# Optimization experiments

Measured on AMD Instinct MI355X. Metric: run time of the kernel, lower is better.

The kernel has to match this reference:

```python
import jax, jax.numpy as jnp
import numpy as np

B, S, H = 4096, 64, 256
NUM_STEPS = 200
DT = 0.01


def setup_inputs() -> dict:
    key = jax.random.key(0)
    ks = jax.random.split(key, 7)
    sc = lambda fan_in: 1.0 / np.sqrt(fan_in)
    return {
        "x0": jax.random.normal(ks[0], (B, S), dtype=jnp.float32),
        "W1": jax.random.normal(ks[1], (S, H), dtype=jnp.float32) * sc(S),
        "b1": jax.random.normal(ks[2], (H,), dtype=jnp.float32) * sc(S),
        "W2": jax.random.normal(ks[3], (H, H), dtype=jnp.float32) * sc(H),
        "b2": jax.random.normal(ks[4], (H,), dtype=jnp.float32) * sc(H),
        "W3": jax.random.normal(ks[5], (H, S), dtype=jnp.float32) * sc(H),
        "b3": jax.random.normal(ks[6], (S,), dtype=jnp.float32) * sc(H),
        "dt_scale": jnp.ones((1,), dtype=jnp.float32) * 0.01,
        "num_steps": NUM_STEPS,
    }


def reference(x0, W1, b1, W2, b2, W3, b3, dt_scale, num_steps):
    # Euler integration of dx/dt = MLP(x); trajectory = [x0, x1, ..., x_num_steps]
    def step(x, _):
        h = jnp.tanh(x @ W1 + b1)          # [B, H]
        h = jnp.tanh(h @ W2 + b2)          # [B, H]
        dx_dt = h @ W3 + b3                # [B, S]
        x_next = x + dx_dt * dt_scale * DT
        return x_next, x_next

    _, traj = jax.lax.scan(step, x0, None, length=num_steps)  # [T, B, S]
    traj = jnp.moveaxis(traj, 0, 1)                            # [B, T, S]
    return jnp.concatenate([x0[:, None, :], traj], axis=1)     # [B, T+1, S]
```

## Files before the change

### kernel.cpp

```cpp
#include <hip/hip_runtime.h>
#include <hip/hip_bf16.h>

typedef __bf16 bf16x8 __attribute__((ext_vector_type(8)));
typedef __bf16 bf16x4 __attribute__((ext_vector_type(4)));
typedef float  f32x4  __attribute__((ext_vector_type(4)));

__device__ __forceinline__ float fast_tanh(float x) {
    float e = __expf(2.0f * x);
    float r = __builtin_amdgcn_rcpf(e + 1.0f);
    return __builtin_fmaf(-2.0f, r, 1.0f);
}

__global__ void prep_weights(const float* __restrict__ W1,
                             const float* __restrict__ W2,
                             const float* __restrict__ W3,
                             __bf16* __restrict__ w1t,
                             __bf16* __restrict__ w2t,
                             __bf16* __restrict__ w3t) {
    int idx = blockIdx.x * blockDim.x + threadIdx.x;
    if (idx < 64 * 256) {
        int n = idx >> 6, k = idx & 63;
        w1t[idx] = (__bf16)W1[k * 256 + n];
    }
    int i2 = idx - 64 * 256;
    if (i2 >= 0 && i2 < 256 * 256) {
        int n = i2 >> 8, k = i2 & 255;
        w2t[i2] = (__bf16)W2[k * 256 + n];
    }
    int i3 = idx - 64 * 256 - 256 * 256;
    if (i3 >= 0 && i3 < 64 * 256) {
        int n = i3 >> 8, k = i3 & 255;
        w3t[i3] = (__bf16)W3[k * 64 + n];
    }
}

__global__ __launch_bounds__(512, 2)
void ode_kernel(const float* __restrict__ x0,
                const float* __restrict__ b1,
                const float* __restrict__ b2,
                const float* __restrict__ b3,
                const float* __restrict__ dt_scale,
                const int*   __restrict__ num_steps,
                const __bf16* __restrict__ w1t,
                const __bf16* __restrict__ w2t,
                const __bf16* __restrict__ w3t,
                float* __restrict__ out) {
    __shared__ float  xs[16][68];
    __shared__ __bf16 xb[16][72];
    __shared__ __bf16 h1[16][264];
    __shared__ __bf16 h2[16][264];

    const int tid  = threadIdx.x;
    const int wave = tid >> 6;
    const int lane = tid & 63;
    const int q    = lane >> 4;
    const int c    = lane & 15;
    const int row0 = blockIdx.x * 16;

    const float scale = dt_scale[0] * 0.01f;
    const int   nT    = num_steps[0];

    bf16x8 w1f[2][2];
    #pragma unroll
    for (int kt = 0; kt < 2; ++kt)
        #pragma unroll
        for (int nt = 0; nt < 2; ++nt) {
            int n = wave * 32 + nt * 16 + c;
            w1f[kt][nt] = *(const bf16x8*)(w1t + n * 64 + kt * 32 + q * 8);
        }
    bf16x8 w2f[8][2];
    #pragma unroll
    for (int kt = 0; kt < 8; ++kt)
        #pragma unroll
        for (int nt = 0; nt < 2; ++nt) {
            int n = wave * 32 + nt * 16 + c;
            w2f[kt][nt] = *(const bf16x8*)(w2t + n * 256 + kt * 32 + q * 8);
        }
    bf16x8 w3f[8];
    f32x4  b3v4 = (f32x4){0.f, 0.f, 0.f, 0.f};
    if (wave < 4) {
        int n = wave * 16 + c;
        #pragma unroll
        for (int kt = 0; kt < 8; ++kt)
            w3f[kt] = *(const bf16x8*)(w3t + n * 256 + kt * 32 + q * 8);
        b3v4 = *(const f32x4*)(b3 + wave * 16 + q * 4);
    }
    f32x4 b1v4[2], b2v4[2];
    #pragma unroll
    for (int nt = 0; nt < 2; ++nt) {
        b1v4[nt] = *(const f32x4*)(b1 + wave * 32 + nt * 16 + q * 4);
        b2v4[nt] = *(const f32x4*)(b2 + wave * 32 + nt * 16 + q * 4);
    }

    const int mio = tid >> 5, sio = (tid & 31) * 2;
    float* outp = out + ((size_t)(row0 + mio) * 201) * 64 + sio;
    {
        const float2 v = *(const float2*)(x0 + (size_t)(row0 + mio) * 64 + sio);
        xs[mio][sio]     = v.x;  xs[mio][sio + 1] = v.y;
        xb[mio][sio]     = (__bf16)v.x;
        xb[mio][sio + 1] = (__bf16)v.y;
        *(float2*)outp = v;
        outp += 64;
    }
    __syncthreads();

    for (int t = 0; t < nT; ++t) {
        {
            f32x4 acc[2] = {b1v4[0], b1v4[1]};
            #pragma unroll
            for (int kt = 0; kt < 2; ++kt) {
                bf16x8 a = *(const bf16x8*)(&xb[c][kt * 32 + q * 8]);
                acc[0] = __builtin_amdgcn_mfma_f32_16x16x32_bf16(w1f[kt][0], a, acc[0], 0, 0, 0);
                acc[1] = __builtin_amdgcn_mfma_f32_16x16x32_bf16(w1f[kt][1], a, acc[1], 0, 0, 0);
            }
            #pragma unroll
            for (int nt = 0; nt < 2; ++nt) {
                bf16x4 o;
                #pragma unroll
                for (int r = 0; r < 4; ++r) o[r] = (__bf16)fast_tanh(acc[nt][r]);
                *(bf16x4*)(&h1[c][wave * 32 + nt * 16 + q * 4]) = o;
            }
        }
        __syncthreads();

        {
            f32x4 acc[2]  = {b2v4[0], b2v4[1]};
            f32x4 accB[2] = {(f32x4){0,0,0,0}, (f32x4){0,0,0,0}};
            #pragma unroll
            for (int kt = 0; kt < 4; ++kt) {
                bf16x8 a0 = *(const bf16x8*)(&h1[c][kt * 32 + q * 8]);
                bf16x8 a1 = *(const bf16x8*)(&h1[c][(kt + 4) * 32 + q * 8]);
                acc[0]  = __builtin_amdgcn_mfma_f32_16x16x32_bf16(w2f[kt][0],     a0, acc[0],  0, 0, 0);
                acc[1]  = __builtin_amdgcn_mfma_f32_16x16x32_bf16(w2f[kt][1],     a0, acc[1],  0, 0, 0);
                accB[0] = __builtin_amdgcn_mfma_f32_16x16x32_bf16(w2f[kt + 4][0], a1, accB[0], 0, 0, 0);
                accB[1] = __builtin_amdgcn_mfma_f32_16x16x32_bf16(w2f[kt + 4][1], a1, accB[1], 0, 0, 0);
            }
            #pragma unroll
            for (int nt = 0; nt < 2; ++nt) {
                f32x4 s = acc[nt] + accB[nt];
                bf16x4 o;
                #pragma unroll
                for (int r = 0; r < 4; ++r) o[r] = (__bf16)fast_tanh(s[r]);
                *(bf16x4*)(&h2[c][wave * 32 + nt * 16 + q * 4]) = o;
            }
        }
        __syncthreads();

        if (wave < 4) {
            f32x4 acc  = b3v4;
            f32x4 accB = (f32x4){0, 0, 0, 0};
            #pragma unroll
            for (int kt = 0; kt < 4; ++kt) {
                bf16x8 a0 = *(const bf16x8*)(&h2[c][kt * 32 + q * 8]);
                bf16x8 a1 = *(const bf16x8*)(&h2[c][(kt + 4) * 32 + q * 8]);
                acc  = __builtin_amdgcn_mfma_f32_16x16x32_bf16(w3f[kt],     a0, acc,  0, 0, 0);
                accB = __builtin_amdgcn_mfma_f32_16x16x32_bf16(w3f[kt + 4], a1, accB, 0, 0, 0);
            }
            acc += accB;
            f32x4 xv = *(f32x4*)(&xs[c][wave * 16 + q * 4]);
            xv += acc * scale;
            *(f32x4*)(&xs[c][wave * 16 + q * 4]) = xv;
            bf16x4 xbv;
            #pragma unroll
            for (int r = 0; r < 4; ++r) xbv[r] = (__bf16)xv[r];
            *(bf16x4*)(&xb[c][wave * 16 + q * 4]) = xbv;
        }
        __syncthreads();

        {
            float2 v = *(const float2*)(&xs[mio][sio]);
            *(float2*)outp = v;
            outp += 64;
        }
    }
}

extern "C" void kernel_launch(void* const* d_in, const int* in_sizes, int n_in,
                              void* d_out, int out_size, void* d_ws, size_t ws_size,
                              hipStream_t stream) {
    const float* x0 = (const float*)d_in[0];
    const float* W1 = (const float*)d_in[1];
    const float* b1 = (const float*)d_in[2];
    const float* W2 = (const float*)d_in[3];
    const float* b2 = (const float*)d_in[4];
    const float* W3 = (const float*)d_in[5];
    const float* b3 = (const float*)d_in[6];
    const float* dt = (const float*)d_in[7];
    const int*   ns = (const int*)d_in[8];

    __bf16* w1t = (__bf16*)d_ws;
    __bf16* w2t = w1t + 64 * 256;
    __bf16* w3t = w2t + 256 * 256;

    prep_weights<<<384, 256, 0, stream>>>(W1, W2, W3, w1t, w2t, w3t);

    int rows = in_sizes[0] / 64;
    ode_kernel<<<rows / 16, 512, 0, stream>>>(x0, b1, b2, b3, dt, ns,
                                              w1t, w2t, w3t, (float*)d_out);
}
```

Baseline: 440.1 us.

## Fold W3 into W1 to carry layer-1 preactivation across steps, dropping a barrier

Precomputes W31 = W3·W1 and c31 = b3·W1 so that the layer-1 preactivation y = xW1 is updated directly each step as y += scale·(h2·W31 + c31), removing the per-step x→h1 matmul phase and one __syncthreads. The dx output projection with W3 is spread across all 8 waves as split-K halves written to shared memory and summed during the output write, and x is kept in registers. Each step now runs a 256x256 matmul instead of the 64x256 layer-1 matmul, and it keeps an extra 256x256 bf16 weight set in registers. The recurrence for y accumulates bf16 rounding error separately from x, so x and y can drift apart over 200 steps.

```diff
diff --git a/kernel.cpp b/kernel.cpp
--- a/kernel.cpp
+++ b/kernel.cpp
@@ -34,6 +34,24 @@
     }
 }
 
+__global__ void prep_w31(const float* __restrict__ W1,
+                         const float* __restrict__ W3,
+                         const float* __restrict__ b3,
+                         __bf16* __restrict__ w31t,
+                         float*  __restrict__ c31) {
+    int idx = blockIdx.x * blockDim.x + threadIdx.x;
+    int k = idx & 255, n = idx >> 8;
+    float acc = 0.f;
+    #pragma unroll 8
+    for (int j = 0; j < 64; ++j) acc += W3[k * 64 + j] * W1[j * 256 + n];
+    w31t[n * 256 + k] = (__bf16)acc;
+    if (idx < 256) {
+        float a = 0.f;
+        for (int j = 0; j < 64; ++j) a += b3[j] * W1[j * 256 + idx];
+        c31[idx] = a;
+    }
+}
+
 __global__ __launch_bounds__(512, 2)
 void ode_kernel(const float* __restrict__ x0,
                 const float* __restrict__ b1,
@@ -44,11 +62,12 @@
                 const __bf16* __restrict__ w1t,
                 const __bf16* __restrict__ w2t,
                 const __bf16* __restrict__ w3t,
+                const __bf16* __restrict__ w31t,
+                const float*  __restrict__ c31,
                 float* __restrict__ out) {
-    __shared__ float  xs[16][68];
-    __shared__ __bf16 xb[16][72];
-    __shared__ __bf16 h1[16][264];
-    __shared__ __bf16 h2[16][264];
+    __shared__ __align__(16) __bf16 h1[16][264];
+    __shared__ __align__(16) __bf16 h2[16][264];
+    __shared__ __align__(16) float  dxp[2][16][68];
 
     const int tid  = threadIdx.x;
     const int wave = tid >> 6;
@@ -57,72 +76,78 @@
     const int c    = lane & 15;
     const int row0 = blockIdx.x * 16;
 
+    const int tileN = (wave & 3) * 16;
+    const int khalf = wave >> 2;
+
     const float scale = dt_scale[0] * 0.01f;
     const int   nT    = num_steps[0];
 
-    bf16x8 w1f[2][2];
+    f32x4 b1v4[2], b2v4[2], c31v[2];
     #pragma unroll
-    for (int kt = 0; kt < 2; ++kt)
+    for (int nt = 0; nt < 2; ++nt) {
+        b1v4[nt] = *(const f32x4*)(b1  + wave * 32 + nt * 16 + q * 4);
+        b2v4[nt] = *(const f32x4*)(b2  + wave * 32 + nt * 16 + q * 4);
+        c31v[nt] = *(const f32x4*)(c31 + wave * 32 + nt * 16 + q * 4);
+    }
+
+    const int mio = tid >> 5, sio = (tid & 31) * 2;
+    float* outp = out + ((size_t)(row0 + mio) * 201) * 64 + sio;
+    float2 xv = *(const float2*)(x0 + (size_t)(row0 + mio) * 64 + sio);
+    const float2 b3v = {b3[sio], b3[sio + 1]};
+    *(float2*)outp = xv;
+    outp += 64;
+
+    f32x4 yv[2];
+    {
+        bf16x8 xf[2];
+        #pragma unroll
+        for (int kt = 0; kt < 2; ++kt) {
+            const float* px = x0 + (size_t)(row0 + c) * 64 + kt * 32 + q * 8;
+            float4 lo = *(const float4*)(px);
+            float4 hi = *(const float4*)(px + 4);
+            xf[kt][0] = (__bf16)lo.x; xf[kt][1] = (__bf16)lo.y;
+            xf[kt][2] = (__bf16)lo.z; xf[kt][3] = (__bf16)lo.w;
+            xf[kt][4] = (__bf16)hi.x; xf[kt][5] = (__bf16)hi.y;
+            xf[kt][6] = (__bf16)hi.z; xf[kt][7] = (__bf16)hi.w;
+        }
+        yv[0] = (f32x4){0.f, 0.f, 0.f, 0.f};
+        yv[1] = (f32x4){0.f, 0.f, 0.f, 0.f};
+        #pragma unroll
+        for (int kt = 0; kt < 2; ++kt)
+            #pragma unroll
+            for (int nt = 0; nt < 2; ++nt) {
+                int n = wave * 32 + nt * 16 + c;
+                bf16x8 w1f = *(const bf16x8*)(w1t + n * 64 + kt * 32 + q * 8);
+                yv[nt] = __builtin_amdgcn_mfma_f32_16x16x32_bf16(w1f, xf[kt], yv[nt], 0, 0, 0);
+            }
+        #pragma unroll
+        for (int nt = 0; nt < 2; ++nt) {
+            bf16x4 o;
+            #pragma unroll
+            for (int r = 0; r < 4; ++r) o[r] = (__bf16)fast_tanh(yv[nt][r] + b1v4[nt][r]);
+            *(bf16x4*)(&h1[c][wave * 32 + nt * 16 + q * 4]) = o;
+        }
+    }
+
+    bf16x8 w2f[8][2], w31f[8][2];
+    #pragma unroll
+    for (int kt = 0; kt < 8; ++kt)
         #pragma unroll
         for (int nt = 0; nt < 2; ++nt) {
             int n = wave * 32 + nt * 16 + c;
-            w1f[kt][nt] = *(const bf16x8*)(w1t + n * 64 + kt * 32 + q * 8);
-        }
-    bf16x8 w2f[8][2];
+            w2f[kt][nt]  = *(const bf16x8*)(w2t  + n * 256 + kt * 32 + q * 8);
+            w31f[kt][nt] = *(const bf16x8*)(w31t + n * 256 + kt * 32 + q * 8);
+        }
+    bf16x8 w3f[4];
     #pragma unroll
-    for (int kt = 0; kt < 8; ++kt)
-        #pragma unroll
-        for (int nt = 0; nt < 2; ++nt) {
-            int n = wave * 32 + nt * 16 + c;
-            w2f[kt][nt] = *(const bf16x8*)(w2t + n * 256 + kt * 32 + q * 8);
-        }
-    bf16x8 w3f[8];
-    f32x4  b3v4 = (f32x4){0.f, 0.f, 0.f, 0.f};
-    if (wave < 4) {
-        int n = wave * 16 + c;
-        #pragma unroll
-        for (int kt = 0; kt < 8; ++kt)
-            w3f[kt] = *(const bf16x8*)(w3t + n * 256 + kt * 32 + q * 8);
-        b3v4 = *(const f32x4*)(b3 + wave * 16 + q * 4);
-    }
-    f32x4 b1v4[2], b2v4[2];
-    #pragma unroll
-    for (int nt = 0; nt < 2; ++nt) {
-        b1v4[nt] = *(const f32x4*)(b1 + wave * 32 + nt * 16 + q * 4);
-        b2v4[nt] = *(const f32x4*)(b2 + wave * 32 + nt * 16 + q * 4);
-    }
-
-    const int mio = tid >> 5, sio = (tid & 31) * 2;
-    float* outp = out + ((size_t)(row0 + mio) * 201) * 64 + sio;
-    {
-        const float2 v = *(const float2*)(x0 + (size_t)(row0 + mio) * 64 + sio);
-        xs[mio][sio]     = v.x;  xs[mio][sio + 1] = v.y;
-        xb[mio][sio]     = (__bf16)v.x;
-        xb[mio][sio + 1] = (__bf16)v.y;
-        *(float2*)outp = v;
-        outp += 64;
-    }
+    for (int kk = 0; kk < 4; ++kk) {
+        int n = tileN + c;
+        w3f[kk] = *(const bf16x8*)(w3t + n * 256 + (khalf * 4 + kk) * 32 + q * 8);
+    }
+
     __syncthreads();
 
     for (int t = 0; t < nT; ++t) {
-        {
-            f32x4 acc[2] = {b1v4[0], b1v4[1]};
-            #pragma unroll
-            for (int kt = 0; kt < 2; ++kt) {
-                bf16x8 a = *(const bf16x8*)(&xb[c][kt * 32 + q * 8]);
-                acc[0] = __builtin_amdgcn_mfma_f32_16x16x32_bf16(w1f[kt][0], a, acc[0], 0, 0, 0);
-                acc[1] = __builtin_amdgcn_mfma_f32_16x16x32_bf16(w1f[kt][1], a, acc[1], 0, 0, 0);
-            }
-            #pragma unroll
-            for (int nt = 0; nt < 2; ++nt) {
-                bf16x4 o;
-                #pragma unroll
-                for (int r = 0; r < 4; ++r) o[r] = (__bf16)fast_tanh(acc[nt][r]);
-                *(bf16x4*)(&h1[c][wave * 32 + nt * 16 + q * 4]) = o;
-            }
-        }
-        __syncthreads();
-
         {
             f32x4 acc[2]  = {b2v4[0], b2v4[1]};
             f32x4 accB[2] = {(f32x4){0,0,0,0}, (f32x4){0,0,0,0}};
@@ -146,30 +171,66 @@
         }
         __syncthreads();
 
-        if (wave < 4) {
-            f32x4 acc  = b3v4;
-            f32x4 accB = (f32x4){0, 0, 0, 0};
-            #pragma unroll
-            for (int kt = 0; kt < 4; ++kt) {
-                bf16x8 a0 = *(const bf16x8*)(&h2[c][kt * 32 + q * 8]);
-                bf16x8 a1 = *(const bf16x8*)(&h2[c][(kt + 4) * 32 + q * 8]);
-                acc  = __builtin_amdgcn_mfma_f32_16x16x32_bf16(w3f[kt],     a0, acc,  0, 0, 0);
-                accB = __builtin_amdgcn_mfma_f32_16x16x32_bf16(w3f[kt + 4], a1, accB, 0, 0, 0);
-            }
-            acc += accB;
-            f32x4 xv = *(f32x4*)(&xs[c][wave * 16 + q * 4]);
-            xv += acc * scale;
-            *(f32x4*)(&xs[c][wave * 16 + q * 4]) = xv;
-            bf16x4 xbv;
-            #pragma unroll
-            for (int r = 0; r < 4; ++r) xbv[r] = (__bf16)xv[r];
-            *(bf16x4*)(&xb[c][wave * 16 + q * 4]) = xbv;
+        {
+            f32x4 accY[2]  = {c31v[0], c31v[1]};
+            f32x4 accYB[2] = {(f32x4){0,0,0,0}, (f32x4){0,0,0,0}};
+            f32x4 accX     = (f32x4){0, 0, 0, 0};
+
+            bf16x8 f0 = *(const bf16x8*)(&h2[c][0 * 32 + q * 8]);
+            bf16x8 f1 = *(const bf16x8*)(&h2[c][1 * 32 + q * 8]);
+            bf16x8 f2 = *(const bf16x8*)(&h2[c][2 * 32 + q * 8]);
+            bf16x8 f3 = *(const bf16x8*)(&h2[c][3 * 32 + q * 8]);
+            accY[0]  = __builtin_amdgcn_mfma_f32_16x16x32_bf16(w31f[0][0], f0, accY[0],  0, 0, 0);
+            accY[1]  = __builtin_amdgcn_mfma_f32_16x16x32_bf16(w31f[0][1], f0, accY[1],  0, 0, 0);
+            accYB[0] = __builtin_amdgcn_mfma_f32_16x16x32_bf16(w31f[1][0], f1, accYB[0], 0, 0, 0);
+            accYB[1] = __builtin_amdgcn_mfma_f32_16x16x32_bf16(w31f[1][1], f1, accYB[1], 0, 0, 0);
+            accY[0]  = __builtin_amdgcn_mfma_f32_16x16x32_bf16(w31f[2][0], f2, accY[0],  0, 0, 0);
+            accY[1]  = __builtin_amdgcn_mfma_f32_16x16x32_bf16(w31f[2][1], f2, accY[1],  0, 0, 0);
+            accYB[0] = __builtin_amdgcn_mfma_f32_16x16x32_bf16(w31f[3][0], f3, accYB[0], 0, 0, 0);
+            accYB[1] = __builtin_amdgcn_mfma_f32_16x16x32_bf16(w31f[3][1], f3, accYB[1], 0, 0, 0);
+            if (khalf == 0) {
+                accX = __builtin_amdgcn_mfma_f32_16x16x32_bf16(w3f[0], f0, accX, 0, 0, 0);
+                accX = __builtin_amdgcn_mfma_f32_16x16x32_bf16(w3f[1], f1, accX, 0, 0, 0);
+                accX = __builtin_amdgcn_mfma_f32_16x16x32_bf16(w3f[2], f2, accX, 0, 0, 0);
+                accX = __builtin_amdgcn_mfma_f32_16x16x32_bf16(w3f[3], f3, accX, 0, 0, 0);
+            }
+            bf16x8 f4 = *(const bf16x8*)(&h2[c][4 * 32 + q * 8]);
+            bf16x8 f5 = *(const bf16x8*)(&h2[c][5 * 32 + q * 8]);
+            bf16x8 f6 = *(const bf16x8*)(&h2[c][6 * 32 + q * 8]);
+            bf16x8 f7 = *(const bf16x8*)(&h2[c][7 * 32 + q * 8]);
+            accY[0]  = __builtin_amdgcn_mfma_f32_16x16x32_bf16(w31f[4][0], f4, accY[0],  0, 0, 0);
+            accY[1]  = __builtin_amdgcn_mfma_f32_16x16x32_bf16(w31f[4][1], f4, accY[1],  0, 0, 0);
+            accYB[0] = __builtin_amdgcn_mfma_f32_16x16x32_bf16(w31f[5][0], f5, accYB[0], 0, 0, 0);
+            accYB[1] = __builtin_amdgcn_mfma_f32_16x16x32_bf16(w31f[5][1], f5, accYB[1], 0, 0, 0);
+            accY[0]  = __builtin_amdgcn_mfma_f32_16x16x32_bf16(w31f[6][0], f6, accY[0],  0, 0, 0);
+            accY[1]  = __builtin_amdgcn_mfma_f32_16x16x32_bf16(w31f[6][1], f6, accY[1],  0, 0, 0);
+            accYB[0] = __builtin_amdgcn_mfma_f32_16x16x32_bf16(w31f[7][0], f7, accYB[0], 0, 0, 0);
+            accYB[1] = __builtin_amdgcn_mfma_f32_16x16x32_bf16(w31f[7][1], f7, accYB[1], 0, 0, 0);
+            if (khalf == 1) {
+                accX = __builtin_amdgcn_mfma_f32_16x16x32_bf16(w3f[0], f4, accX, 0, 0, 0);
+                accX = __builtin_amdgcn_mfma_f32_16x16x32_bf16(w3f[1], f5, accX, 0, 0, 0);
+                accX = __builtin_amdgcn_mfma_f32_16x16x32_bf16(w3f[2], f6, accX, 0, 0, 0);
+                accX = __builtin_amdgcn_mfma_f32_16x16x32_bf16(w3f[3], f7, accX, 0, 0, 0);
+            }
+
+            #pragma unroll
+            for (int nt = 0; nt < 2; ++nt) {
+                yv[nt] += (accY[nt] + accYB[nt]) * scale;
+                bf16x4 o;
+                #pragma unroll
+                for (int r = 0; r < 4; ++r) o[r] = (__bf16)fast_tanh(yv[nt][r] + b1v4[nt][r]);
+                *(bf16x4*)(&h1[c][wave * 32 + nt * 16 + q * 4]) = o;
+            }
+            *(f32x4*)(&dxp[khalf][c][tileN + q * 4]) = accX;
         }
         __syncthreads();
 
         {
-            float2 v = *(const float2*)(&xs[mio][sio]);
-            *(float2*)outp = v;
+            float2 d0 = *(const float2*)(&dxp[0][mio][sio]);
+            float2 d1 = *(const float2*)(&dxp[1][mio][sio]);
+            xv.x += scale * (d0.x + d1.x + b3v.x);
+            xv.y += scale * (d0.y + d1.y + b3v.y);
+            *(float2*)outp = xv;
             outp += 64;
         }
     }
@@ -188,13 +249,17 @@
     const float* dt = (const float*)d_in[7];
     const int*   ns = (const int*)d_in[8];
 
-    __bf16* w1t = (__bf16*)d_ws;
-    __bf16* w2t = w1t + 64 * 256;
-    __bf16* w3t = w2t + 256 * 256;
+    __bf16* w1t  = (__bf16*)d_ws;
+    __bf16* w2t  = w1t + 64 * 256;
+    __bf16* w3t  = w2t + 256 * 256;
+    __bf16* w31t = w3t + 64 * 256;
+    float*  c31  = (float*)(w31t + 256 * 256);
 
     prep_weights<<<384, 256, 0, stream>>>(W1, W2, W3, w1t, w2t, w3t);
+    prep_w31<<<256, 256, 0, stream>>>(W1, W3, b3, w31t, c31);
 
     int rows = in_sizes[0] / 64;
     ode_kernel<<<rows / 16, 512, 0, stream>>>(x0, b1, b2, b3, dt, ns,
-                                              w1t, w2t, w3t, (float*)d_out);
-}
+                                              w1t, w2t, w3t, w31t, c31,
+                                              (float*)d_out);
+}
```

Result: slower. 468.6 us (+6.5%).
